# Performance work log

Measured on AMD Instinct MI355X. Metric: run time of the kernel, lower is better.

The kernel has to match this reference:

```python
import jax, jax.numpy as jnp
import numpy as np

N_HEAD = 32


def _apply_rope(x, rope):
    # x: (B, H, T, hs); rope: (block_size, hs//2) angles
    B, H, T, hs = x.shape
    ang = rope[:T]  # (T, hs//2)
    cos = jnp.cos(ang)[None, :, None, :]  # (1, T, 1, hs//2)
    sin = jnp.sin(ang)[None, :, None, :]
    xt = x.transpose(0, 2, 1, 3).reshape(B, T, H, hs // 2, 2)
    x0, x1 = xt[..., 0], xt[..., 1]
    out_r = x0 * cos - x1 * sin
    out_i = x0 * sin + x1 * cos
    out = jnp.stack([out_r, out_i], axis=-1).reshape(B, T, H, hs)
    return out.transpose(0, 2, 1, 3)


def setup_inputs() -> dict:
    key = jax.random.key(0)
    ks = jax.random.split(key, 6)
    B, T, C = 2, 2048, 4096
    aT = 10
    hs = C // N_HEAD
    return {
        "x": jax.random.normal(ks[0], (B, T, C), dtype=jnp.float32),
        "adaption_prompt": jax.random.normal(ks[1], (1, aT, C), dtype=jnp.float32),
        "rope_cache": jax.random.uniform(ks[2], (4096, hs // 2), dtype=jnp.float32) * 2.0 * np.pi,
        "w_attn": jax.random.normal(ks[3], (C, 3 * C), dtype=jnp.float32) * 0.02,
        "w_proj": jax.random.normal(ks[4], (C, C), dtype=jnp.float32) * 0.02,
        "gating_factor": jax.random.normal(ks[5], (1,), dtype=jnp.float32) * 0.1,
    }


def reference(x, adaption_prompt, rope_cache, w_attn, w_proj, gating_factor):
    B, T, C = x.shape
    H = N_HEAD
    hs = C // H

    qkv = x @ w_attn  # (B, T, 3C)
    q, k, v = jnp.split(qkv, 3, axis=2)
    q = q.reshape(B, T, H, hs).transpose(0, 2, 1, 3)  # (B, H, T, hs)
    k = k.reshape(B, T, H, hs).transpose(0, 2, 1, 3)
    v = v.reshape(B, T, H, hs).transpose(0, 2, 1, 3)

    q = _apply_rope(q, rope_cache)
    k = _apply_rope(k, rope_cache)

    # causal SDPA, scale = 1/sqrt(head_size)
    scale = 1.0 / jnp.sqrt(jnp.asarray(hs, dtype=q.dtype))
    scores = jnp.einsum("bhqd,bhkd->bhqk", q, k) * scale
    causal = jnp.tril(jnp.ones((T, T), dtype=bool))
    scores = jnp.where(causal[None, None, :, :], scores, jnp.asarray(-jnp.inf, scores.dtype))
    attn = jax.nn.softmax(scores, axis=-1)
    y = jnp.einsum("bhqk,bhkd->bhqd", attn, v)  # (B, H, T, hs)

    # adapter attention (note: scale uses full n_embd, as in source)
    aT = adaption_prompt.shape[1]
    aqkv = adaption_prompt @ w_attn  # (1, aT, 3C)
    _, ak, av = jnp.split(aqkv, 3, axis=2)
    ak = ak.reshape(1, aT, H, hs).transpose(0, 2, 1, 3)  # (1, H, aT, hs)
    av = av.reshape(1, aT, H, hs).transpose(0, 2, 1, 3)
    ascores = jnp.einsum("bhqd,xhkd->bhqk", q, ak) / jnp.sqrt(jnp.asarray(C, q.dtype))
    ascores = gating_factor[0] * jax.nn.softmax(ascores.astype(jnp.float32), axis=-1).astype(q.dtype)
    y = y + jnp.einsum("bhqk,xhkd->bhqd", ascores, av)

    y = y.transpose(0, 2, 1, 3).reshape(B, T, C)
    return y @ w_proj
```

## Files before the change

### kernel.cpp

```cpp
#include <hip/hip_runtime.h>

typedef unsigned short u16;
typedef unsigned int u32;
typedef __attribute__((ext_vector_type(4))) float f32x4;
typedef __attribute__((ext_vector_type(8))) _Float16 half8;
typedef __attribute__((ext_vector_type(8))) unsigned short u16x8;
typedef __attribute__((ext_vector_type(4))) unsigned short u16x4;

static __device__ __forceinline__ u16 f2h(float f) {
  union { _Float16 h; u16 u; } c;
  c.h = (_Float16)f;
  return c.u;
}
static __device__ __forceinline__ float h2f(u16 u) {
  union { _Float16 h; u16 u; } c;
  c.u = u;
  return (float)c.h;
}
static __device__ __forceinline__ void gload_lds16(const void* g, void* l) {
  __builtin_amdgcn_global_load_lds((const __attribute__((address_space(1))) void*)g,
                                   (__attribute__((address_space(3))) void*)l,
                                   16, 0, 0);
}

__global__ __launch_bounds__(256) void transpose_cvt(const float* __restrict__ src,
                                                     u16* __restrict__ dst,
                                                     int R, int C) {
  __shared__ float tile[32][33];
  const int tx = threadIdx.x, ty = threadIdx.y;
  const int c0 = blockIdx.x << 5, r0 = blockIdx.y << 5;
#pragma unroll
  for (int i = 0; i < 32; i += 8)
    tile[ty + i][tx] = src[(size_t)(r0 + ty + i) * C + c0 + tx];
  __syncthreads();
#pragma unroll
  for (int i = 0; i < 32; i += 8)
    dst[(size_t)(c0 + ty + i) * R + r0 + tx] = f2h(tile[tx][ty + i]);
}

__global__ __launch_bounds__(256) void cvt_f32_f16(const float* __restrict__ in,
                                                   u16* __restrict__ out, int n4) {
  int i = blockIdx.x * 256 + threadIdx.x;
  if (i >= n4) return;
  f32x4 v = *(const f32x4*)(in + (size_t)i * 4);
  u16x4 o;
  o[0] = f2h(v[0]); o[1] = f2h(v[1]); o[2] = f2h(v[2]); o[3] = f2h(v[3]);
  *(u16x4*)(out + (size_t)i * 4) = o;
}

static __device__ __forceinline__ void store_out(float* C, size_t idx, float v) { C[idx] = v; }
static __device__ __forceinline__ void store_out(u16* C, size_t idx, float v) { C[idx] = f2h(v); }

static __device__ __forceinline__ void stageA(const u16* __restrict__ Ab, int K, int kt,
                                              u16* As, int mh, int t) {
  int hf = t >> 8;
  int tt = t & 255;
  int row = hf * 128 + mh * 32 + (tt >> 3);
  int slot = tt & 7;
  gload_lds16(Ab + (size_t)row * K + kt + ((slot ^ (row & 7)) << 3),
              (char*)As + hf * 16384 + mh * 4096 + tt * 16);
}
static __device__ __forceinline__ void stageB(const u16* __restrict__ Bb, int K, int kt,
                                              u16* Bs, int j, int t) {
  int row = j * 64 + (t >> 3);
  int slot = t & 7;
  gload_lds16(Bb + (size_t)row * K + kt + ((slot ^ (row & 7)) << 3),
              (char*)Bs + j * 8192 + t * 16);
}

#define LOAD_BF(BS)                                                              \
  _Pragma("unroll") for (int nf = 0; nf < 4; ++nf)                               \
    _Pragma("unroll") for (int kk = 0; kk < 2; ++kk) {                           \
      int row = wn * 64 + nf * 16 + l15;                                         \
      int slot = (kk * 4 + g) ^ (l15 & 7);                                       \
      bf[nf][kk] = *(const half8*)((const char*)(BS) + row * 128 + slot * 16);   \
    }

#define LOAD_AF(AF, AS, Q)                                                       \
  _Pragma("unroll") for (int mf = 0; mf < 2; ++mf)                               \
    _Pragma("unroll") for (int kk = 0; kk < 2; ++kk) {                           \
      int row = wm * 128 + ((Q) * 2 + mf) * 16 + l15;                            \
      int slot = (kk * 4 + g) ^ (l15 & 7);                                       \
      (AF)[mf][kk] = *(const half8*)((const char*)(AS) + row * 128 + slot * 16); \
    }

#define MFMA_BURST(AF, Q)                                                        \
  __builtin_amdgcn_s_setprio(1);                                                 \
  _Pragma("unroll") for (int kk = 0; kk < 2; ++kk)                               \
    _Pragma("unroll") for (int mf = 0; mf < 2; ++mf)                             \
      _Pragma("unroll") for (int nf = 0; nf < 4; ++nf)                           \
        acc[(Q) * 2 + mf][nf] = __builtin_amdgcn_mfma_f32_16x16x32_f16(          \
            (AF)[mf][kk], bf[nf][kk], acc[(Q) * 2 + mf][nf], 0, 0, 0);           \
  __builtin_amdgcn_s_setprio(0);

template <typename OutT>
__global__ __launch_bounds__(512, 2) void gemm256(const u16* __restrict__ A,
                                                  const u16* __restrict__ Bt,
                                                  OutT* __restrict__ C,
                                                  int M, int N, int K, int nbn) {
  __shared__ u16 lds[4][16384];
  const int t = threadIdx.x;
  const int lane = t & 63;
  const int wid = t >> 6;
  const int g = lane >> 4, l15 = lane & 15;
  const int wm = wid >> 2, wn = wid & 3;
  const int nwg = gridDim.x;
  const int bid = blockIdx.x;
  const int wgid = (bid & 7) * (nwg >> 3) + (bid >> 3);
  const int bm = wgid / nbn, bn = wgid % nbn;
  const u16* Ab = A + (size_t)bm * 256 * K;
  const u16* Bb = Bt + (size_t)bn * 256 * K;
  f32x4 acc[8][4] = {};

  stageA(Ab, K, 0, lds[0], 0, t);
  stageA(Ab, K, 0, lds[0], 1, t);
  stageA(Ab, K, 0, lds[0], 2, t);
  stageA(Ab, K, 0, lds[0], 3, t);
  stageB(Bb, K, 0, lds[1], 0, t);
  stageB(Bb, K, 0, lds[1], 1, t);
  stageB(Bb, K, 0, lds[1], 2, t);
  stageB(Bb, K, 0, lds[1], 3, t);
  asm volatile("s_waitcnt vmcnt(0)" ::: "memory");
  __builtin_amdgcn_s_barrier();

  const int nt = K >> 6;
  for (int i = 0; i < nt; ++i) {
    u16* As  = lds[(i & 1) << 1];
    u16* Bs  = lds[((i & 1) << 1) + 1];
    u16* Asn = lds[((i + 1) & 1) << 1];
    u16* Bsn = lds[(((i + 1) & 1) << 1) + 1];
    int k1 = (i + 1) << 6; if (k1 >= K) k1 = 0;
    half8 bf[4][2], afA[2][2], afB[2][2];
    LOAD_BF(Bs);
    LOAD_AF(afA, As, 0);
    stageB(Bb, K, k1, Bsn, 0, t);
    stageB(Bb, K, k1, Bsn, 1, t);
    stageB(Bb, K, k1, Bsn, 2, t);
    stageB(Bb, K, k1, Bsn, 3, t);
    stageA(Ab, K, k1, Asn, 0, t);
    stageA(Ab, K, k1, Asn, 1, t);
    stageA(Ab, K, k1, Asn, 2, t);
    stageA(Ab, K, k1, Asn, 3, t);
    LOAD_AF(afB, As, 1);
    MFMA_BURST(afA, 0);
    LOAD_AF(afA, As, 2);
    MFMA_BURST(afB, 1);
    LOAD_AF(afB, As, 3);
    MFMA_BURST(afA, 2);
    MFMA_BURST(afB, 3);
    asm volatile("s_waitcnt vmcnt(0) lgkmcnt(0)" ::: "memory");
    __builtin_amdgcn_s_barrier();
  }

#pragma unroll
  for (int mf = 0; mf < 8; ++mf) {
    int row0 = bm * 256 + wm * 128 + mf * 16 + 4 * g;
#pragma unroll
    for (int nf = 0; nf < 4; ++nf) {
      int col = bn * 256 + wn * 64 + nf * 16 + l15;
#pragma unroll
      for (int r = 0; r < 4; ++r)
        store_out(C, (size_t)(row0 + r) * N + col, acc[mf][nf][r]);
    }
  }
}

__global__ __launch_bounds__(256) void rope_kernel(u16* __restrict__ qkv,
                                                   const float* __restrict__ rope) {
  int idx = blockIdx.x * 256 + threadIdx.x;
  int bt = idx >> 12;
  int pp = idx & 4095;
  int part = pp >> 11;
  int within = pp & 2047;
  int hh = within >> 6;
  int p = within & 63;
  int tpos = bt & 2047;
  size_t off = (size_t)bt * 12288 + part * 4096 + hh * 128 + 2 * p;
  u32* ptr = (u32*)(qkv + off);
  u32 v = *ptr;
  float x0 = h2f((u16)(v & 0xffff));
  float x1 = h2f((u16)(v >> 16));
  float sn, cs;
  __sincosf(rope[tpos * 64 + p], &sn, &cs);
  float y0 = x0 * cs - x1 * sn;
  float y1 = x0 * sn + x1 * cs;
  *ptr = (u32)f2h(y0) | ((u32)f2h(y1) << 16);
}

__global__ __launch_bounds__(256) void v_transpose(const u16* __restrict__ qkv,
                                                   u16* __restrict__ vt) {
  __shared__ u16 tile[64 * 128];
  const int bx = blockIdx.x;
  const int tt = bx & 31, h = (bx >> 5) & 31, b = bx >> 10;
  const u16* src = qkv + (size_t)b * 2048 * 12288 + 8192 + h * 128;
  const int t = threadIdx.x;
#pragma unroll
  for (int i = 0; i < 4; ++i) {
    int c = t + 256 * i;
    int row = c >> 4, slot = c & 15;
    u16x8 v = *(const u16x8*)(src + (size_t)(tt * 64 + row) * 12288 + slot * 8);
    *(u16x8*)(tile + row * 128 + ((slot ^ (row >> 3)) << 3)) = v;
  }
  __syncthreads();
  u16* dst = vt + (size_t)(b * 32 + h) * 128 * 2048 + tt * 64;
#pragma unroll
  for (int i = 0; i < 4; ++i) {
    int c = t + 256 * i;
    int drow = c >> 3, t8 = c & 7;
    u16x8 o;
#pragma unroll
    for (int e = 0; e < 8; ++e) {
      int row = t8 * 8 + e;
      int slot = (drow >> 3) ^ (row >> 3);
      o[e] = tile[row * 128 + (slot << 3) + (drow & 7)];
    }
    *(u16x8*)(dst + (size_t)drow * 2048 + t8 * 8) = o;
  }
}

__global__ __launch_bounds__(256) void adaption_kv_kernel(const float* __restrict__ prompt,
                                                          const float* __restrict__ w_attn,
                                                          u16* __restrict__ akbuf,
                                                          u16* __restrict__ avbuf) {
  __shared__ float pl[10][512];
  __shared__ float red[8][10][32];
  const int t = threadIdx.x;
  const int tc = t & 31, tk = t >> 5;
  const int n = blockIdx.x * 32 + tc;
  float acc[10] = {};
  for (int k0 = 0; k0 < 4096; k0 += 512) {
    __syncthreads();
#pragma unroll
    for (int i = 0; i < 20; ++i) {
      int idx = t + 256 * i;
      int j = idx >> 9, kk = idx & 511;
      pl[j][kk] = prompt[(size_t)j * 4096 + k0 + kk];
    }
    __syncthreads();
    for (int kk = tk; kk < 512; kk += 8) {
      float wv = w_attn[(size_t)(k0 + kk) * 12288 + 4096 + n];
#pragma unroll
      for (int j = 0; j < 10; ++j) acc[j] += pl[j][kk] * wv;
    }
  }
  __syncthreads();
#pragma unroll
  for (int j = 0; j < 10; ++j) red[tk][j][tc] = acc[j];
  __syncthreads();
  if (tk == 0) {
    float s[10];
#pragma unroll
    for (int j = 0; j < 10; ++j) {
      s[j] = 0.f;
#pragma unroll
      for (int q = 0; q < 8; ++q) s[j] += red[q][j][tc];
    }
    u16* dst;
    int hh, d;
    if (n < 4096) { dst = akbuf; hh = n >> 7; d = n & 127; }
    else          { dst = avbuf; hh = (n - 4096) >> 7; d = n & 127; }
#pragma unroll
    for (int j = 0; j < 16; ++j)
      dst[(size_t)(hh * 16 + j) * 128 + d] = (j < 10) ? f2h(s[j]) : (u16)0;
  }
}

__global__ __launch_bounds__(256) void attn_kernel(const u16* __restrict__ qkv,
                                                   const u16* __restrict__ vt,
                                                   const u16* __restrict__ akbuf,
                                                   const u16* __restrict__ avbuf,
                                                   const float* __restrict__ gating,
                                                   u16* __restrict__ y) {
  __shared__ u16 Kl[64 * 128];
  __shared__ u16 Vtl[128 * 64];
  __shared__ u16 Pl[4][16 * 64];

  const int t = threadIdx.x;
  const int lane = t & 63, w = t >> 6;
  const int g = lane >> 4, l15 = lane & 15;
  const int bx = blockIdx.x;
  const int qb = 31 - (bx >> 6);
  const int bh = bx & 63, b = bh >> 5, h = bh & 31;
  const int ldq = 12288;
  const u16* Qg = qkv + (size_t)b * 2048 * ldq + h * 128;
  const u16* Kg = Qg + 4096;
  const u16* VtG = vt + (size_t)(b * 32 + h) * 128 * 2048;
  u16* AKb = &Pl[0][0];

#pragma unroll
  for (int i = 0; i < 4; ++i) {
    int c = t + 256 * i;
    int row = c >> 4, slot = c & 15;
    gload_lds16(Qg + (size_t)(qb * 64 + row) * ldq + ((slot ^ (row & 15)) << 3),
                (char*)Kl + c * 16);
  }
  {
    int row = t >> 4, slot = t & 15;
    gload_lds16(akbuf + (size_t)(h * 16 + row) * 128 + ((slot ^ row) << 3),
                (char*)AKb + t * 16);
  }
  __syncthreads();

  half8 qf[4];
#pragma unroll
  for (int kk = 0; kk < 4; ++kk) {
    int slot = (kk * 4 + g) ^ l15;
    qf[kk] = *(const half8*)((const char*)Kl + (w * 16 + l15) * 256 + (slot << 4));
  }
  f32x4 sa = {};
#pragma unroll
  for (int kk = 0; kk < 4; ++kk) {
    int slot = (kk * 4 + g) ^ l15;
    half8 af = *(const half8*)((const char*)AKb + l15 * 256 + (slot << 4));
    sa = __builtin_amdgcn_mfma_f32_16x16x32_f16(qf[kk], af, sa, 0, 0, 0);
  }
  __syncthreads();

  f32x4 acc[8] = {};
  float mrun[4], lrun[4];
#pragma unroll
  for (int r = 0; r < 4; ++r) { mrun[r] = -1e30f; lrun[r] = 0.f; }

  for (int kvt = 0; kvt <= qb; ++kvt) {
#pragma unroll
    for (int i = 0; i < 4; ++i) {
      int c = t + 256 * i;
      int row = c >> 4, slot = c & 15;
      gload_lds16(Kg + (size_t)(kvt * 64 + row) * ldq + ((slot ^ (row & 15)) << 3),
                  (char*)Kl + c * 16);
    }
#pragma unroll
    for (int i = 0; i < 4; ++i) {
      int c = t + 256 * i;
      int d = c >> 3, s3 = c & 7;
      gload_lds16(VtG + (size_t)d * 2048 + kvt * 64 + ((s3 ^ (d & 7)) << 3),
                  (char*)Vtl + c * 16);
    }
    __syncthreads();

    f32x4 s[4] = {};
#pragma unroll
    for (int nf = 0; nf < 4; ++nf) {
#pragma unroll
      for (int kk = 0; kk < 4; ++kk) {
        int slot = (kk * 4 + g) ^ l15;
        half8 kf = *(const half8*)((const char*)Kl + (nf * 16 + l15) * 256 + (slot << 4));
        s[nf] = __builtin_amdgcn_mfma_f32_16x16x32_f16(qf[kk], kf, s[nf], 0, 0, 0);
      }
    }
    const float sc = 0.08838834764831843f;
    if (kvt == qb) {
#pragma unroll
      for (int nf = 0; nf < 4; ++nf)
#pragma unroll
        for (int r = 0; r < 4; ++r) {
          int kv = nf * 16 + l15;
          int qq = w * 16 + 4 * g + r;
          float v = s[nf][r] * sc;
          s[nf][r] = (kv <= qq) ? v : -1e30f;
        }
    } else {
#pragma unroll
      for (int nf = 0; nf < 4; ++nf)
#pragma unroll
        for (int r = 0; r < 4; ++r) s[nf][r] *= sc;
    }

    float alpha[4];
#pragma unroll
    for (int r = 0; r < 4; ++r) {
      float mt = fmaxf(fmaxf(s[0][r], s[1][r]), fmaxf(s[2][r], s[3][r]));
#pragma unroll
      for (int off = 1; off < 16; off <<= 1)
        mt = fmaxf(mt, __shfl_xor(mt, off, 64));
      float mn = fmaxf(mrun[r], mt);
      alpha[r] = __expf(mrun[r] - mn);
      mrun[r] = mn;
      float rs = 0.f;
#pragma unroll
      for (int nf = 0; nf < 4; ++nf) {
        float p = __expf(s[nf][r] - mn);
        s[nf][r] = p;
        rs += p;
      }
#pragma unroll
      for (int off = 1; off < 16; off <<= 1)
        rs += __shfl_xor(rs, off, 64);
      lrun[r] = lrun[r] * alpha[r] + rs;
    }
#pragma unroll
    for (int nd = 0; nd < 8; ++nd)
#pragma unroll
      for (int r = 0; r < 4; ++r)
        acc[nd][r] *= alpha[r];

#pragma unroll
    for (int nf = 0; nf < 4; ++nf)
#pragma unroll
      for (int r = 0; r < 4; ++r) {
        int qq = 4 * g + r;
        int kv = nf * 16 + l15;
        int byteoff = (qq * 128 + kv * 2) ^ ((qq & 7) << 4);
        *(u16*)((char*)Pl[w] + byteoff) = f2h(s[nf][r]);
      }

#pragma unroll
    for (int kk2 = 0; kk2 < 2; ++kk2) {
      int pslot = (kk2 * 4 + g) ^ (l15 & 7);
      half8 pf = *(const half8*)((const char*)Pl[w] + l15 * 128 + (pslot << 4));
#pragma unroll
      for (int nd = 0; nd < 8; ++nd) {
        int d = nd * 16 + l15;
        int slot = (kk2 * 4 + g) ^ (d & 7);
        half8 vf = *(const half8*)((const char*)Vtl + d * 128 + (slot << 4));
        acc[nd] = __builtin_amdgcn_mfma_f32_16x16x32_f16(pf, vf, acc[nd], 0, 0, 0);
      }
    }
    __syncthreads();
  }

  {
    int d = t >> 1;
    int jb = (t & 1) << 4;
#pragma unroll
    for (int i = 0; i < 16; ++i) {
      int j = jb + i;
      u16 v = (j < 16) ? avbuf[(size_t)(h * 16 + j) * 128 + d] : (u16)0;
      int byteoff = (d * 64 + j * 2) ^ ((d & 3) << 4);
      *(u16*)((char*)Kl + byteoff) = v;
    }
  }
  __syncthreads();

  float ga = gating[0];
  float pa4[4];
#pragma unroll
  for (int r = 0; r < 4; ++r) {
    float v = sa[r] * (1.0f / 64.0f);
    if (l15 >= 10) v = -1e30f;
    float mt = v;
#pragma unroll
    for (int off = 1; off < 16; off <<= 1)
      mt = fmaxf(mt, __shfl_xor(mt, off, 64));
    float p = __expf(v - mt);
    float rs = p;
#pragma unroll
    for (int off = 1; off < 16; off <<= 1)
      rs += __shfl_xor(rs, off, 64);
    pa4[r] = p / rs * ga;
  }
#pragma unroll
  for (int r = 0; r < 4; ++r) {
    float inv = 1.0f / lrun[r];
#pragma unroll
    for (int nd = 0; nd < 8; ++nd)
      acc[nd][r] *= inv;
  }
#pragma unroll
  for (int r = 0; r < 4; ++r) {
    int qq = 4 * g + r;
    int b1 = (qq * 128 + l15 * 2) ^ ((qq & 7) << 4);
    *(u16*)((char*)Pl[w] + b1) = f2h(pa4[r]);
    int b2 = (qq * 128 + (16 + l15) * 2) ^ ((qq & 7) << 4);
    *(u16*)((char*)Pl[w] + b2) = 0;
  }
  {
    int pslot = g ^ (l15 & 7);
    half8 pf = *(const half8*)((const char*)Pl[w] + l15 * 128 + (pslot << 4));
#pragma unroll
    for (int nd = 0; nd < 8; ++nd) {
      int d = nd * 16 + l15;
      int byteoff = (d * 64 + g * 16) ^ ((d & 3) << 4);
      half8 avf = *(const half8*)((const char*)Kl + byteoff);
      acc[nd] = __builtin_amdgcn_mfma_f32_16x16x32_f16(pf, avf, acc[nd], 0, 0, 0);
    }
  }
#pragma unroll
  for (int nd = 0; nd < 8; ++nd) {
    int col = h * 128 + nd * 16 + l15;
#pragma unroll
    for (int r = 0; r < 4; ++r) {
      int row = qb * 64 + w * 16 + 4 * g + r;
      y[(size_t)(b * 2048 + row) * 4096 + col] = f2h(acc[nd][r]);
    }
  }
}

extern "C" void kernel_launch(void* const* d_in, const int* in_sizes, int n_in,
                              void* d_out, int out_size, void* d_ws, size_t ws_size,
                              hipStream_t stream) {
  (void)in_sizes; (void)n_in; (void)out_size; (void)ws_size;
  const float* x      = (const float*)d_in[0];
  const float* prompt = (const float*)d_in[1];
  const float* rope   = (const float*)d_in[2];
  const float* w_attn = (const float*)d_in[3];
  const float* w_proj = (const float*)d_in[4];
  const float* gating = (const float*)d_in[5];
  float* out = (float*)d_out;

  char* ws = (char*)d_ws;
  u16* WtA = (u16*)(ws);
  u16* Yb  = (u16*)(ws);
  u16* VtG = (u16*)(ws + 33554432);
  u16* qkv = (u16*)(ws + 100663296);
  u16* xb  = (u16*)(ws + 201326592);
  u16* WtP = (u16*)(ws + 201326592);
  u16* akb = (u16*)(ws + 234881024);
  u16* avb = (u16*)(ws + 234881024 + 131072);

  transpose_cvt<<<dim3(384, 128), dim3(32, 8), 0, stream>>>(w_attn, WtA, 4096, 12288);
  cvt_f32_f16<<<dim3(16384), dim3(256), 0, stream>>>(x, xb, 4194304);
  gemm256<u16><<<dim3(768), dim3(512), 0, stream>>>(xb, WtA, qkv, 4096, 12288, 4096, 48);
  rope_kernel<<<dim3(65536), dim3(256), 0, stream>>>(qkv, rope);
  v_transpose<<<dim3(2048), dim3(256), 0, stream>>>(qkv, VtG);
  adaption_kv_kernel<<<dim3(256), dim3(256), 0, stream>>>(prompt, w_attn, akb, avb);
  attn_kernel<<<dim3(2048), dim3(256), 0, stream>>>(qkv, VtG, akb, avb, gating, Yb);
  transpose_cvt<<<dim3(128, 128), dim3(32, 8), 0, stream>>>(w_proj, WtP, 4096, 4096);
  gemm256<float><<<dim3(256), dim3(512), 0, stream>>>(Yb, WtP, out, 4096, 4096, 4096, 16);
}
```

Before: 999.4 us.

## Double-buffer attention KV tiles with 128-row query blocks and vectorized transpose

The attention kernel now uses 512 threads covering 128 query rows per block. K/V tiles are double-buffered in LDS so the next tile's global-to-LDS loads overlap the current tile's MFMA work, and the old syncthreads are replaced with explicit waitcnt plus barrier. Query blocks are interleaved long/short to balance causal work across the grid. Softmax row reductions use DPP for the first two steps, and the weight transpose-convert kernel moves to 64x64 tiles with vector loads and stores. The larger blocks and doubled LDS footprint may lower occupancy, and the interleaved block ordering changes tail behaviour.

New measurement: 1.094 ms. +9.5%, slower.

```diff
diff --git a/kernel.cpp b/kernel.cpp
--- a/kernel.cpp
+++ b/kernel.cpp
@@ -23,19 +23,50 @@
                                    16, 0, 0);
 }
 
+template <int CTRL>
+static __device__ __forceinline__ float dppf(float x) {
+  int i = __float_as_int(x);
+  int r = __builtin_amdgcn_update_dpp(i, i, CTRL, 0xf, 0xf, true);
+  return __int_as_float(r);
+}
+static __device__ __forceinline__ float red16_max(float v) {
+  v = fmaxf(v, dppf<0xB1>(v));
+  v = fmaxf(v, dppf<0x4E>(v));
+  v = fmaxf(v, __shfl_xor(v, 4, 64));
+  v = fmaxf(v, __shfl_xor(v, 8, 64));
+  return v;
+}
+static __device__ __forceinline__ float red16_sum(float v) {
+  v += dppf<0xB1>(v);
+  v += dppf<0x4E>(v);
+  v += __shfl_xor(v, 4, 64);
+  v += __shfl_xor(v, 8, 64);
+  return v;
+}
+
 __global__ __launch_bounds__(256) void transpose_cvt(const float* __restrict__ src,
                                                      u16* __restrict__ dst,
                                                      int R, int C) {
-  __shared__ float tile[32][33];
-  const int tx = threadIdx.x, ty = threadIdx.y;
-  const int c0 = blockIdx.x << 5, r0 = blockIdx.y << 5;
-#pragma unroll
-  for (int i = 0; i < 32; i += 8)
-    tile[ty + i][tx] = src[(size_t)(r0 + ty + i) * C + c0 + tx];
+  __shared__ float tt[64][65];
+  const int t = threadIdx.x;
+  const int c0 = blockIdx.x << 6, r0 = blockIdx.y << 6;
+  const int r = t >> 4, cb = (t & 15) << 2;
+#pragma unroll
+  for (int i = 0; i < 4; ++i) {
+    f32x4 v = *(const f32x4*)(src + (size_t)(r0 + r + i * 16) * C + c0 + cb);
+#pragma unroll
+    for (int j = 0; j < 4; ++j) tt[cb + j][r + i * 16] = v[j];
+  }
   __syncthreads();
-#pragma unroll
-  for (int i = 0; i < 32; i += 8)
-    dst[(size_t)(c0 + ty + i) * R + r0 + tx] = f2h(tile[tx][ty + i]);
+  const int cc = t >> 2, r8 = (t & 3) << 4;
+  u16x8 o0, o1;
+#pragma unroll
+  for (int j = 0; j < 8; ++j) o0[j] = f2h(tt[cc][r8 + j]);
+#pragma unroll
+  for (int j = 0; j < 8; ++j) o1[j] = f2h(tt[cc][r8 + 8 + j]);
+  u16* dp = dst + (size_t)(c0 + cc) * R + r0 + r8;
+  *(u16x8*)dp = o0;
+  *(u16x8*)(dp + 8) = o1;
 }
 
 __global__ __launch_bounds__(256) void cvt_f32_f16(const float* __restrict__ in,
@@ -265,97 +296,120 @@
   }
 }
 
-__global__ __launch_bounds__(256) void attn_kernel(const u16* __restrict__ qkv,
-                                                   const u16* __restrict__ vt,
-                                                   const u16* __restrict__ akbuf,
-                                                   const u16* __restrict__ avbuf,
-                                                   const float* __restrict__ gating,
-                                                   u16* __restrict__ y) {
-  __shared__ u16 Kl[64 * 128];
-  __shared__ u16 Vtl[128 * 64];
-  __shared__ u16 Pl[4][16 * 64];
+__global__ __launch_bounds__(512, 4) void attn_kernel(const u16* __restrict__ qkv,
+                                                      const u16* __restrict__ vt,
+                                                      const u16* __restrict__ akbuf,
+                                                      const u16* __restrict__ avbuf,
+                                                      const float* __restrict__ gating,
+                                                      u16* __restrict__ y) {
+  __shared__ u16 Kb[2][64 * 128];
+  __shared__ u16 Vb[2][128 * 64];
+  __shared__ u16 Pl[8][1024];
 
   const int t = threadIdx.x;
   const int lane = t & 63, w = t >> 6;
   const int g = lane >> 4, l15 = lane & 15;
   const int bx = blockIdx.x;
-  const int qb = 31 - (bx >> 6);
+  const int p = bx >> 6;
+  const int qb = (p & 1) ? (15 - (p >> 1)) : (p >> 1);
   const int bh = bx & 63, b = bh >> 5, h = bh & 31;
   const int ldq = 12288;
   const u16* Qg = qkv + (size_t)b * 2048 * ldq + h * 128;
   const u16* Kg = Qg + 4096;
   const u16* VtG = vt + (size_t)(b * 32 + h) * 128 * 2048;
-  u16* AKb = &Pl[0][0];
 
 #pragma unroll
   for (int i = 0; i < 4; ++i) {
-    int c = t + 256 * i;
+    int c = t + 512 * i;
     int row = c >> 4, slot = c & 15;
-    gload_lds16(Qg + (size_t)(qb * 64 + row) * ldq + ((slot ^ (row & 15)) << 3),
-                (char*)Kl + c * 16);
-  }
-  {
+    gload_lds16(Qg + (size_t)(qb * 128 + row) * ldq + ((slot ^ (row & 15)) << 3),
+                (char*)Kb[0] + c * 16);
+  }
+  if (t < 256) {
     int row = t >> 4, slot = t & 15;
     gload_lds16(akbuf + (size_t)(h * 16 + row) * 128 + ((slot ^ row) << 3),
-                (char*)AKb + t * 16);
-  }
-  __syncthreads();
+                (char*)Pl[0] + t * 16);
+  }
+  asm volatile("s_waitcnt vmcnt(0)" ::: "memory");
+  __builtin_amdgcn_s_barrier();
 
   half8 qf[4];
+  const char* Qbase = (const char*)Kb[0] + (w >> 2) * 16384;
+#pragma unroll
+  for (int kk = 0; kk < 4; ++kk) {
+    int row = (w & 3) * 16 + l15;
+    int slot = (kk * 4 + g) ^ l15;
+    qf[kk] = *(const half8*)(Qbase + row * 256 + (slot << 4));
+  }
+  f32x4 sa = {};
 #pragma unroll
   for (int kk = 0; kk < 4; ++kk) {
     int slot = (kk * 4 + g) ^ l15;
-    qf[kk] = *(const half8*)((const char*)Kl + (w * 16 + l15) * 256 + (slot << 4));
-  }
-  f32x4 sa = {};
-#pragma unroll
-  for (int kk = 0; kk < 4; ++kk) {
-    int slot = (kk * 4 + g) ^ l15;
-    half8 af = *(const half8*)((const char*)AKb + l15 * 256 + (slot << 4));
+    half8 af = *(const half8*)((const char*)Pl[0] + l15 * 256 + (slot << 4));
     sa = __builtin_amdgcn_mfma_f32_16x16x32_f16(qf[kk], af, sa, 0, 0, 0);
   }
-  __syncthreads();
+  asm volatile("s_waitcnt lgkmcnt(0)" ::: "memory");
+  __builtin_amdgcn_s_barrier();
+
+#pragma unroll
+  for (int i = 0; i < 2; ++i) {
+    int c = t + 512 * i;
+    int row = c >> 4, slot = c & 15;
+    gload_lds16(Kg + (size_t)row * ldq + ((slot ^ (row & 15)) << 3),
+                (char*)Kb[0] + c * 16);
+  }
+#pragma unroll
+  for (int i = 0; i < 2; ++i) {
+    int c = t + 512 * i;
+    int d = c >> 3, s3 = c & 7;
+    gload_lds16(VtG + (size_t)d * 2048 + ((s3 ^ (d & 7)) << 3),
+                (char*)Vb[0] + c * 16);
+  }
+  asm volatile("s_waitcnt vmcnt(0)" ::: "memory");
+  __builtin_amdgcn_s_barrier();
 
   f32x4 acc[8] = {};
   float mrun[4], lrun[4];
 #pragma unroll
   for (int r = 0; r < 4; ++r) { mrun[r] = -1e30f; lrun[r] = 0.f; }
-
-  for (int kvt = 0; kvt <= qb; ++kvt) {
-#pragma unroll
-    for (int i = 0; i < 4; ++i) {
-      int c = t + 256 * i;
+  const int last = 2 * qb + 1;
+  const int dt = 2 * qb + (w >> 2);
+
+  for (int kvt = 0; kvt <= last; ++kvt) {
+    const int cur = kvt & 1;
+    const int kn = (kvt < last) ? (kvt + 1) : (kvt - 1);
+    const int nb = cur ^ 1;
+#pragma unroll
+    for (int i = 0; i < 2; ++i) {
+      int c = t + 512 * i;
       int row = c >> 4, slot = c & 15;
-      gload_lds16(Kg + (size_t)(kvt * 64 + row) * ldq + ((slot ^ (row & 15)) << 3),
-                  (char*)Kl + c * 16);
-    }
-#pragma unroll
-    for (int i = 0; i < 4; ++i) {
-      int c = t + 256 * i;
+      gload_lds16(Kg + (size_t)(kn * 64 + row) * ldq + ((slot ^ (row & 15)) << 3),
+                  (char*)Kb[nb] + c * 16);
+    }
+#pragma unroll
+    for (int i = 0; i < 2; ++i) {
+      int c = t + 512 * i;
       int d = c >> 3, s3 = c & 7;
-      gload_lds16(VtG + (size_t)d * 2048 + kvt * 64 + ((s3 ^ (d & 7)) << 3),
-                  (char*)Vtl + c * 16);
-    }
-    __syncthreads();
-
+      gload_lds16(VtG + (size_t)d * 2048 + kn * 64 + ((s3 ^ (d & 7)) << 3),
+                  (char*)Vb[nb] + c * 16);
+    }
     f32x4 s[4] = {};
 #pragma unroll
-    for (int nf = 0; nf < 4; ++nf) {
+    for (int nf = 0; nf < 4; ++nf)
 #pragma unroll
       for (int kk = 0; kk < 4; ++kk) {
         int slot = (kk * 4 + g) ^ l15;
-        half8 kf = *(const half8*)((const char*)Kl + (nf * 16 + l15) * 256 + (slot << 4));
+        half8 kf = *(const half8*)((const char*)Kb[cur] + (nf * 16 + l15) * 256 + (slot << 4));
         s[nf] = __builtin_amdgcn_mfma_f32_16x16x32_f16(qf[kk], kf, s[nf], 0, 0, 0);
       }
-    }
     const float sc = 0.08838834764831843f;
-    if (kvt == qb) {
+    if (kvt >= dt) {
 #pragma unroll
       for (int nf = 0; nf < 4; ++nf)
 #pragma unroll
         for (int r = 0; r < 4; ++r) {
-          int kv = nf * 16 + l15;
-          int qq = w * 16 + 4 * g + r;
+          int kv = kvt * 64 + nf * 16 + l15;
+          int qq = qb * 128 + w * 16 + 4 * g + r;
           float v = s[nf][r] * sc;
           s[nf][r] = (kv <= qq) ? v : -1e30f;
         }
@@ -365,35 +419,28 @@
 #pragma unroll
         for (int r = 0; r < 4; ++r) s[nf][r] *= sc;
     }
-
     float alpha[4];
 #pragma unroll
     for (int r = 0; r < 4; ++r) {
       float mt = fmaxf(fmaxf(s[0][r], s[1][r]), fmaxf(s[2][r], s[3][r]));
-#pragma unroll
-      for (int off = 1; off < 16; off <<= 1)
-        mt = fmaxf(mt, __shfl_xor(mt, off, 64));
+      mt = red16_max(mt);
       float mn = fmaxf(mrun[r], mt);
       alpha[r] = __expf(mrun[r] - mn);
       mrun[r] = mn;
       float rs = 0.f;
 #pragma unroll
       for (int nf = 0; nf < 4; ++nf) {
-        float p = __expf(s[nf][r] - mn);
-        s[nf][r] = p;
-        rs += p;
+        float pv = __expf(s[nf][r] - mn);
+        s[nf][r] = pv;
+        rs += pv;
       }
-#pragma unroll
-      for (int off = 1; off < 16; off <<= 1)
-        rs += __shfl_xor(rs, off, 64);
+      rs = red16_sum(rs);
       lrun[r] = lrun[r] * alpha[r] + rs;
     }
 #pragma unroll
     for (int nd = 0; nd < 8; ++nd)
 #pragma unroll
-      for (int r = 0; r < 4; ++r)
-        acc[nd][r] *= alpha[r];
-
+      for (int r = 0; r < 4; ++r) acc[nd][r] *= alpha[r];
 #pragma unroll
     for (int nf = 0; nf < 4; ++nf)
 #pragma unroll
@@ -403,7 +450,6 @@
         int byteoff = (qq * 128 + kv * 2) ^ ((qq & 7) << 4);
         *(u16*)((char*)Pl[w] + byteoff) = f2h(s[nf][r]);
       }
-
 #pragma unroll
     for (int kk2 = 0; kk2 < 2; ++kk2) {
       int pslot = (kk2 * 4 + g) ^ (l15 & 7);
@@ -412,25 +458,27 @@
       for (int nd = 0; nd < 8; ++nd) {
         int d = nd * 16 + l15;
         int slot = (kk2 * 4 + g) ^ (d & 7);
-        half8 vf = *(const half8*)((const char*)Vtl + d * 128 + (slot << 4));
+        half8 vf = *(const half8*)((const char*)Vb[cur] + d * 128 + (slot << 4));
         acc[nd] = __builtin_amdgcn_mfma_f32_16x16x32_f16(pf, vf, acc[nd], 0, 0, 0);
       }
     }
-    __syncthreads();
+    asm volatile("s_waitcnt vmcnt(0) lgkmcnt(0)" ::: "memory");
+    __builtin_amdgcn_s_barrier();
   }
 
   {
-    int d = t >> 1;
-    int jb = (t & 1) << 4;
-#pragma unroll
-    for (int i = 0; i < 16; ++i) {
+    int d = t >> 2;
+    int jb = (t & 3) << 3;
+#pragma unroll
+    for (int i = 0; i < 8; ++i) {
       int j = jb + i;
       u16 v = (j < 16) ? avbuf[(size_t)(h * 16 + j) * 128 + d] : (u16)0;
       int byteoff = (d * 64 + j * 2) ^ ((d & 3) << 4);
-      *(u16*)((char*)Kl + byteoff) = v;
-    }
-  }
-  __syncthreads();
+      *(u16*)((char*)Kb[0] + byteoff) = v;
+    }
+  }
+  asm volatile("s_waitcnt lgkmcnt(0)" ::: "memory");
+  __builtin_amdgcn_s_barrier();
 
   float ga = gating[0];
   float pa4[4];
@@ -438,23 +486,16 @@
   for (int r = 0; r < 4; ++r) {
     float v = sa[r] * (1.0f / 64.0f);
     if (l15 >= 10) v = -1e30f;
-    float mt = v;
-#pragma unroll
-    for (int off = 1; off < 16; off <<= 1)
-      mt = fmaxf(mt, __shfl_xor(mt, off, 64));
-    float p = __expf(v - mt);
-    float rs = p;
-#pragma unroll
-    for (int off = 1; off < 16; off <<= 1)
-      rs += __shfl_xor(rs, off, 64);
-    pa4[r] = p / rs * ga;
+    float mt = red16_max(v);
+    float pv = __expf(v - mt);
+    float rs = red16_sum(pv);
+    pa4[r] = pv / rs * ga;
   }
 #pragma unroll
   for (int r = 0; r < 4; ++r) {
     float inv = 1.0f / lrun[r];
 #pragma unroll
-    for (int nd = 0; nd < 8; ++nd)
-      acc[nd][r] *= inv;
+    for (int nd = 0; nd < 8; ++nd) acc[nd][r] *= inv;
   }
 #pragma unroll
   for (int r = 0; r < 4; ++r) {
@@ -471,7 +512,7 @@
     for (int nd = 0; nd < 8; ++nd) {
       int d = nd * 16 + l15;
       int byteoff = (d * 64 + g * 16) ^ ((d & 3) << 4);
-      half8 avf = *(const half8*)((const char*)Kl + byteoff);
+      half8 avf = *(const half8*)((const char*)Kb[0] + byteoff);
       acc[nd] = __builtin_amdgcn_mfma_f32_16x16x32_f16(pf, avf, acc[nd], 0, 0, 0);
     }
   }
@@ -480,7 +521,7 @@
     int col = h * 128 + nd * 16 + l15;
 #pragma unroll
     for (int r = 0; r < 4; ++r) {
-      int row = qb * 64 + w * 16 + 4 * g + r;
+      int row = qb * 128 + w * 16 + 4 * g + r;
       y[(size_t)(b * 2048 + row) * 4096 + col] = f2h(acc[nd][r]);
     }
   }
@@ -508,13 +549,13 @@
   u16* akb = (u16*)(ws + 234881024);
   u16* avb = (u16*)(ws + 234881024 + 131072);
 
-  transpose_cvt<<<dim3(384, 128), dim3(32, 8), 0, stream>>>(w_attn, WtA, 4096, 12288);
+  transpose_cvt<<<dim3(192, 64), dim3(256), 0, stream>>>(w_attn, WtA, 4096, 12288);
   cvt_f32_f16<<<dim3(16384), dim3(256), 0, stream>>>(x, xb, 4194304);
   gemm256<u16><<<dim3(768), dim3(512), 0, stream>>>(xb, WtA, qkv, 4096, 12288, 4096, 48);
   rope_kernel<<<dim3(65536), dim3(256), 0, stream>>>(qkv, rope);
   v_transpose<<<dim3(2048), dim3(256), 0, stream>>>(qkv, VtG);
   adaption_kv_kernel<<<dim3(256), dim3(256), 0, stream>>>(prompt, w_attn, akb, avb);
-  attn_kernel<<<dim3(2048), dim3(256), 0, stream>>>(qkv, VtG, akb, avb, gating, Yb);
-  transpose_cvt<<<dim3(128, 128), dim3(32, 8), 0, stream>>>(w_proj, WtP, 4096, 4096);
+  attn_kernel<<<dim3(1024), dim3(512), 0, stream>>>(qkv, VtG, akb, avb, gating, Yb);
+  transpose_cvt<<<dim3(64, 64), dim3(256), 0, stream>>>(w_proj, WtP, 4096, 4096);
   gemm256<float><<<dim3(256), dim3(512), 0, stream>>>(Yb, WtP, out, 4096, 4096, 4096, 16);
 }
```

## Fuse V transpose into QKV GEMM epilogue and vectorize weight transpose

Applied to the files above, without the earlier changes.

The QKV GEMM epilogue now writes the V third of its output directly in transposed per-head layout (b,h,d,t) and writes Q/K into a narrower buffer, which removes the separate v_transpose kernel and its read/write pass over V. The weight transpose-convert kernel is rewritten to use 64x64 tiles with vectorized float4 loads and 16-byte fp16 stores. In exchange, the V epilogue issues strided 8-byte stores across rows of 2048, which coalesce poorly.

After: 985.5 us. About the same (-1.4%).

```diff
diff --git a/kernel.cpp b/kernel.cpp
--- a/kernel.cpp
+++ b/kernel.cpp
@@ -26,16 +26,26 @@
 __global__ __launch_bounds__(256) void transpose_cvt(const float* __restrict__ src,
                                                      u16* __restrict__ dst,
                                                      int R, int C) {
-  __shared__ float tile[32][33];
-  const int tx = threadIdx.x, ty = threadIdx.y;
-  const int c0 = blockIdx.x << 5, r0 = blockIdx.y << 5;
-#pragma unroll
-  for (int i = 0; i < 32; i += 8)
-    tile[ty + i][tx] = src[(size_t)(r0 + ty + i) * C + c0 + tx];
+  __shared__ float tt[64][65];
+  const int t = threadIdx.x;
+  const int c0 = blockIdx.x << 6, r0 = blockIdx.y << 6;
+  const int r = t >> 4, cb = (t & 15) << 2;
+#pragma unroll
+  for (int i = 0; i < 4; ++i) {
+    f32x4 v = *(const f32x4*)(src + (size_t)(r0 + r + i * 16) * C + c0 + cb);
+#pragma unroll
+    for (int j = 0; j < 4; ++j) tt[cb + j][r + i * 16] = v[j];
+  }
   __syncthreads();
-#pragma unroll
-  for (int i = 0; i < 32; i += 8)
-    dst[(size_t)(c0 + ty + i) * R + r0 + tx] = f2h(tile[tx][ty + i]);
+  const int cc = t >> 2, r8 = (t & 3) << 4;
+  u16x8 o0, o1;
+#pragma unroll
+  for (int j = 0; j < 8; ++j) o0[j] = f2h(tt[cc][r8 + j]);
+#pragma unroll
+  for (int j = 0; j < 8; ++j) o1[j] = f2h(tt[cc][r8 + 8 + j]);
+  u16* dp = dst + (size_t)(c0 + cc) * R + r0 + r8;
+  *(u16x8*)dp = o0;
+  *(u16x8*)(dp + 8) = o1;
 }
 
 __global__ __launch_bounds__(256) void cvt_f32_f16(const float* __restrict__ in,
@@ -97,7 +107,9 @@
 __global__ __launch_bounds__(512, 2) void gemm256(const u16* __restrict__ A,
                                                   const u16* __restrict__ Bt,
                                                   OutT* __restrict__ C,
-                                                  int M, int N, int K, int nbn) {
+                                                  u16* __restrict__ vtg,
+                                                  int M, int N, int K, int nbn,
+                                                  int ldc) {
   __shared__ u16 lds[4][16384];
   const int t = threadIdx.x;
   const int lane = t & 63;
@@ -152,20 +164,37 @@
     __builtin_amdgcn_s_barrier();
   }
 
-#pragma unroll
-  for (int mf = 0; mf < 8; ++mf) {
-    int row0 = bm * 256 + wm * 128 + mf * 16 + 4 * g;
-#pragma unroll
-    for (int nf = 0; nf < 4; ++nf) {
-      int col = bn * 256 + wn * 64 + nf * 16 + l15;
-#pragma unroll
-      for (int r = 0; r < 4; ++r)
-        store_out(C, (size_t)(row0 + r) * N + col, acc[mf][nf][r]);
-    }
-  }
-}
-
-__global__ __launch_bounds__(256) void rope_kernel(u16* __restrict__ qkv,
+  if (vtg && bn >= 32) {
+#pragma unroll
+    for (int mf = 0; mf < 8; ++mf) {
+      int row0 = bm * 256 + wm * 128 + mf * 16 + 4 * g;
+      int bI = row0 >> 11, t0 = row0 & 2047;
+#pragma unroll
+      for (int nf = 0; nf < 4; ++nf) {
+        int vcol = bn * 256 + wn * 64 + nf * 16 + l15 - 8192;
+        int hI = vcol >> 7, dI = vcol & 127;
+        u16x4 o;
+#pragma unroll
+        for (int r = 0; r < 4; ++r) o[r] = f2h(acc[mf][nf][r]);
+        *(u16x4*)(vtg + ((size_t)(bI * 32 + hI) * 128 + dI) * 2048 + t0) = o;
+      }
+    }
+  } else {
+#pragma unroll
+    for (int mf = 0; mf < 8; ++mf) {
+      int row0 = bm * 256 + wm * 128 + mf * 16 + 4 * g;
+#pragma unroll
+      for (int nf = 0; nf < 4; ++nf) {
+        int col = bn * 256 + wn * 64 + nf * 16 + l15;
+#pragma unroll
+        for (int r = 0; r < 4; ++r)
+          store_out(C, (size_t)(row0 + r) * ldc + col, acc[mf][nf][r]);
+      }
+    }
+  }
+}
+
+__global__ __launch_bounds__(256) void rope_kernel(u16* __restrict__ qk,
                                                    const float* __restrict__ rope) {
   int idx = blockIdx.x * 256 + threadIdx.x;
   int bt = idx >> 12;
@@ -175,8 +204,8 @@
   int hh = within >> 6;
   int p = within & 63;
   int tpos = bt & 2047;
-  size_t off = (size_t)bt * 12288 + part * 4096 + hh * 128 + 2 * p;
-  u32* ptr = (u32*)(qkv + off);
+  size_t off = (size_t)bt * 8192 + part * 4096 + hh * 128 + 2 * p;
+  u32* ptr = (u32*)(qk + off);
   u32 v = *ptr;
   float x0 = h2f((u16)(v & 0xffff));
   float x1 = h2f((u16)(v >> 16));
@@ -185,37 +214,6 @@
   float y0 = x0 * cs - x1 * sn;
   float y1 = x0 * sn + x1 * cs;
   *ptr = (u32)f2h(y0) | ((u32)f2h(y1) << 16);
-}
-
-__global__ __launch_bounds__(256) void v_transpose(const u16* __restrict__ qkv,
-                                                   u16* __restrict__ vt) {
-  __shared__ u16 tile[64 * 128];
-  const int bx = blockIdx.x;
-  const int tt = bx & 31, h = (bx >> 5) & 31, b = bx >> 10;
-  const u16* src = qkv + (size_t)b * 2048 * 12288 + 8192 + h * 128;
-  const int t = threadIdx.x;
-#pragma unroll
-  for (int i = 0; i < 4; ++i) {
-    int c = t + 256 * i;
-    int row = c >> 4, slot = c & 15;
-    u16x8 v = *(const u16x8*)(src + (size_t)(tt * 64 + row) * 12288 + slot * 8);
-    *(u16x8*)(tile + row * 128 + ((slot ^ (row >> 3)) << 3)) = v;
-  }
-  __syncthreads();
-  u16* dst = vt + (size_t)(b * 32 + h) * 128 * 2048 + tt * 64;
-#pragma unroll
-  for (int i = 0; i < 4; ++i) {
-    int c = t + 256 * i;
-    int drow = c >> 3, t8 = c & 7;
-    u16x8 o;
-#pragma unroll
-    for (int e = 0; e < 8; ++e) {
-      int row = t8 * 8 + e;
-      int slot = (drow >> 3) ^ (row >> 3);
-      o[e] = tile[row * 128 + (slot << 3) + (drow & 7)];
-    }
-    *(u16x8*)(dst + (size_t)drow * 2048 + t8 * 8) = o;
-  }
 }
 
 __global__ __launch_bounds__(256) void adaption_kv_kernel(const float* __restrict__ prompt,
@@ -265,7 +263,7 @@
   }
 }
 
-__global__ __launch_bounds__(256) void attn_kernel(const u16* __restrict__ qkv,
+__global__ __launch_bounds__(256) void attn_kernel(const u16* __restrict__ qk,
                                                    const u16* __restrict__ vt,
                                                    const u16* __restrict__ akbuf,
                                                    const u16* __restrict__ avbuf,
@@ -281,8 +279,8 @@
   const int bx = blockIdx.x;
   const int qb = 31 - (bx >> 6);
   const int bh = bx & 63, b = bh >> 5, h = bh & 31;
-  const int ldq = 12288;
-  const u16* Qg = qkv + (size_t)b * 2048 * ldq + h * 128;
+  const int ldq = 8192;
+  const u16* Qg = qk + (size_t)b * 2048 * ldq + h * 128;
   const u16* Kg = Qg + 4096;
   const u16* VtG = vt + (size_t)(b * 32 + h) * 128 * 2048;
   u16* AKb = &Pl[0][0];
@@ -501,20 +499,21 @@
   char* ws = (char*)d_ws;
   u16* WtA = (u16*)(ws);
   u16* Yb  = (u16*)(ws);
-  u16* VtG = (u16*)(ws + 33554432);
-  u16* qkv = (u16*)(ws + 100663296);
+  u16* qk  = (u16*)(ws + 100663296);
+  u16* VtG = (u16*)(ws + 167772160);
   u16* xb  = (u16*)(ws + 201326592);
   u16* WtP = (u16*)(ws + 201326592);
   u16* akb = (u16*)(ws + 234881024);
   u16* avb = (u16*)(ws + 234881024 + 131072);
 
-  transpose_cvt<<<dim3(384, 128), dim3(32, 8), 0, stream>>>(w_attn, WtA, 4096, 12288);
+  transpose_cvt<<<dim3(192, 64), dim3(256), 0, stream>>>(w_attn, WtA, 4096, 12288);
   cvt_f32_f16<<<dim3(16384), dim3(256), 0, stream>>>(x, xb, 4194304);
-  gemm256<u16><<<dim3(768), dim3(512), 0, stream>>>(xb, WtA, qkv, 4096, 12288, 4096, 48);
-  rope_kernel<<<dim3(65536), dim3(256), 0, stream>>>(qkv, rope);
-  v_transpose<<<dim3(2048), dim3(256), 0, stream>>>(qkv, VtG);
+  gemm256<u16><<<dim3(768), dim3(512), 0, stream>>>(xb, WtA, qk, VtG,
+                                                    4096, 12288, 4096, 48, 8192);
+  rope_kernel<<<dim3(65536), dim3(256), 0, stream>>>(qk, rope);
   adaption_kv_kernel<<<dim3(256), dim3(256), 0, stream>>>(prompt, w_attn, akb, avb);
-  attn_kernel<<<dim3(2048), dim3(256), 0, stream>>>(qkv, VtG, akb, avb, gating, Yb);
-  transpose_cvt<<<dim3(128, 128), dim3(32, 8), 0, stream>>>(w_proj, WtP, 4096, 4096);
-  gemm256<float><<<dim3(256), dim3(512), 0, stream>>>(Yb, WtP, out, 4096, 4096, 4096, 16);
-}
+  attn_kernel<<<dim3(2048), dim3(256), 0, stream>>>(qk, VtG, akb, avb, gating, Yb);
+  transpose_cvt<<<dim3(64, 64), dim3(256), 0, stream>>>(w_proj, WtP, 4096, 4096);
+  gemm256<float><<<dim3(256), dim3(512), 0, stream>>>(Yb, WtP, out, nullptr,
+                                                      4096, 4096, 4096, 16, 4096);
+}
```
